# Performance work log

Measured on AMD Instinct MI355X. Metric: run time of the kernel, lower is better.

The kernel has to match this reference:

```python
import jax, jax.numpy as jnp
import numpy as np
from jax import lax

B, C_IN, C_OUT, N, R, K = 16, 64, 64, 32768, 32, 3
GROUPS, GN_EPS = 8, 1e-5


def swish(x):
    return x * jax.nn.sigmoid(x)


def group_norm(x, gamma, beta):
    b, c = x.shape[:2]
    xg = x.reshape(b, GROUPS, -1)
    mu = xg.mean(-1, keepdims=True)
    var = xg.var(-1, keepdims=True)
    xn = ((xg - mu) * lax.rsqrt(var + GN_EPS)).reshape(x.shape)
    shp = (1, c) + (1,) * (x.ndim - 2)
    return xn * gamma.reshape(shp) + beta.reshape(shp)


def conv3d(x, w, b):
    y = lax.conv_general_dilated(x, w, (1, 1, 1), 'SAME',
                                 dimension_numbers=('NCDHW', 'OIDHW', 'NCDHW'))
    return y + b.reshape(1, -1, 1, 1, 1)


def voxelize(features, coords):
    # features [B,C,N], coords [B,3,N] -> vox [B,C,R,R,R], norm_coords [B,3,N] in [0,R-1]
    c = coords - coords.mean(axis=2, keepdims=True)
    scale = jnp.linalg.norm(c, axis=1, keepdims=True).max(axis=2, keepdims=True) * 2.0  # eps=0
    norm = jnp.clip((c / scale + 0.5) * R, 0.0, R - 1)
    vc = jnp.round(norm).astype(jnp.int32)
    idx = (vc[:, 0] * R + vc[:, 1]) * R + vc[:, 2]  # [B,N] flat voxel index

    def per_batch(f, i):  # f [C,N], i [N] -> [C, R^3] scatter-average
        sums = jax.ops.segment_sum(f.T, i, num_segments=R ** 3)  # [R^3, C]
        cnt = jax.ops.segment_sum(jnp.ones(i.shape, f.dtype), i, num_segments=R ** 3)
        return (sums / jnp.maximum(cnt, 1.0)[:, None]).T

    vox = jax.vmap(per_batch)(features, idx).reshape(features.shape[0], features.shape[1], R, R, R)
    return vox, norm


def trilinear_devoxelize(vox, coords):
    # vox [B,C,R,R,R], coords [B,3,N] float in [0,R-1] -> [B,C,N]
    b, c = vox.shape[:2]
    flat = vox.reshape(b, c, R ** 3)
    c0f = jnp.floor(coords)
    f = coords - c0f
    i0 = jnp.clip(c0f.astype(jnp.int32), 0, R - 1)
    i1 = jnp.clip(i0 + 1, 0, R - 1)
    out = jnp.zeros((b, c, coords.shape[2]), vox.dtype)
    for xi, wx in ((i0[:, 0], 1.0 - f[:, 0]), (i1[:, 0], f[:, 0])):
        for yi, wy in ((i0[:, 1], 1.0 - f[:, 1]), (i1[:, 1], f[:, 1])):
            for zi, wz in ((i0[:, 2], 1.0 - f[:, 2]), (i1[:, 2], f[:, 2])):
                idx = (xi * R + yi) * R + zi  # [B,N]
                w = (wx * wy * wz)[:, None, :]
                out = out + jnp.take_along_axis(flat, idx[:, None, :], axis=2) * w
    return out


def setup_inputs():
    key = jax.random.key(0)
    ks = jax.random.split(key, 6)
    s1 = 1.0 / np.sqrt(C_IN * K ** 3)
    s2 = 1.0 / np.sqrt(C_OUT * K ** 3)
    sp = 1.0 / np.sqrt(C_IN)
    return {
        'features': jax.random.normal(ks[0], (B, C_IN, N), jnp.float32),
        'coords': jax.random.normal(ks[1], (B, 3, N), jnp.float32),
        'w1': jax.random.normal(ks[2], (C_OUT, C_IN, K, K, K), jnp.float32) * s1,
        'b1': jnp.zeros((C_OUT,), jnp.float32),
        'g1': jnp.ones((C_OUT,), jnp.float32),
        'be1': jnp.zeros((C_OUT,), jnp.float32),
        'w2': jax.random.normal(ks[3], (C_OUT, C_OUT, K, K, K), jnp.float32) * s2,
        'b2': jnp.zeros((C_OUT,), jnp.float32),
        'g2': jnp.ones((C_OUT,), jnp.float32),
        'be2': jnp.zeros((C_OUT,), jnp.float32),
        'wp': jax.random.normal(ks[4], (C_OUT, C_IN), jnp.float32) * sp,
        'bp': jnp.zeros((C_OUT,), jnp.float32),
        'gp': jnp.ones((C_OUT,), jnp.float32),
        'bep': jnp.zeros((C_OUT,), jnp.float32),
    }


def reference(features, coords, w1, b1, g1, be1, w2, b2, g2, be2, wp, bp, gp, bep):
    coords_sg = lax.stop_gradient(coords)  # torch: coords.detach() inside Voxelization
    vox, norm_coords = voxelize(features, coords_sg)
    h = swish(group_norm(conv3d(vox, w1, b1), g1, be1))
    # Dropout(0.1) is identity in eval mode
    h = swish(group_norm(conv3d(h, w2, b2), g2, be2))
    vpts = trilinear_devoxelize(h, norm_coords)
    pf = swish(group_norm(jnp.einsum('oc,bcn->bon', wp, features) + bp[None, :, None], gp, bep))
    return (vpts + pf, coords)
```

## Files before the change

kernel.cpp:

```cpp
#include <hip/hip_runtime.h>
#include <hip/hip_bf16.h>
#include <math.h>

#define BB   16
#define CCH  64
#define NPT  32768
#define RR   32
#define R3   32768
#define GSZ  262144
#define VOXB 2228224

typedef __attribute__((ext_vector_type(8))) short bfx8;
typedef __attribute__((ext_vector_type(8))) unsigned short usx8;
typedef __attribute__((ext_vector_type(16))) float f32x16;

__device__ __forceinline__ short f2bf(float f) {
    unsigned u = __builtin_bit_cast(unsigned, f);
    u += 0x7fff + ((u >> 16) & 1);
    return (short)(u >> 16);
}
__device__ __forceinline__ float bf2f(unsigned short s) {
    unsigned u = ((unsigned)s) << 16;
    return __builtin_bit_cast(float, u);
}

__device__ __forceinline__ int fzswz(int z) {
    return (((z & 3) ^ ((z >> 2) & 3)) << 3);
}

__device__ __forceinline__ float blockReduceSumF(float v) {
    __shared__ float sm[16];
    #pragma unroll
    for (int o = 32; o > 0; o >>= 1) v += __shfl_down(v, o);
    __syncthreads();
    if ((threadIdx.x & 63) == 0) sm[threadIdx.x >> 6] = v;
    __syncthreads();
    float s = 0.f;
    int nw = blockDim.x >> 6;
    for (int i = 0; i < nw; ++i) s += sm[i];
    return s;
}

__device__ __forceinline__ float blockReduceMaxF(float v) {
    __shared__ float sm[16];
    #pragma unroll
    for (int o = 32; o > 0; o >>= 1) v = fmaxf(v, __shfl_down(v, o));
    __syncthreads();
    if ((threadIdx.x & 63) == 0) sm[threadIdx.x >> 6] = v;
    __syncthreads();
    float s = sm[0];
    int nw = blockDim.x >> 6;
    for (int i = 1; i < nw; ++i) s = fmaxf(s, sm[i]);
    return s;
}

__global__ void k_cstat_sum(const float* __restrict__ coords, float* __restrict__ csum) {
    int b = blockIdx.x >> 3, seg = blockIdx.x & 7;
    const float* cb = coords + (size_t)b * 3 * NPT;
    int n0 = seg << 12;
    float sx = 0.f, sy = 0.f, sz = 0.f;
    for (int n = n0 + threadIdx.x; n < n0 + 4096; n += 256) {
        sx += cb[n]; sy += cb[NPT + n]; sz += cb[2 * NPT + n];
    }
    sx = blockReduceSumF(sx);
    sy = blockReduceSumF(sy);
    sz = blockReduceSumF(sz);
    if (threadIdx.x == 0) {
        atomicAdd(&csum[b * 4 + 0], sx);
        atomicAdd(&csum[b * 4 + 1], sy);
        atomicAdd(&csum[b * 4 + 2], sz);
    }
}

__global__ void k_cstat_max(const float* __restrict__ coords, const float* __restrict__ csum,
                            int* __restrict__ cmax) {
    int b = blockIdx.x >> 3, seg = blockIdx.x & 7;
    const float* cb = coords + (size_t)b * 3 * NPT;
    float mx = csum[b * 4 + 0] * (1.f / NPT);
    float my = csum[b * 4 + 1] * (1.f / NPT);
    float mz = csum[b * 4 + 2] * (1.f / NPT);
    int n0 = seg << 12;
    float mn = 0.f;
    for (int n = n0 + threadIdx.x; n < n0 + 4096; n += 256) {
        float x = cb[n] - mx, y = cb[NPT + n] - my, z = cb[2 * NPT + n] - mz;
        mn = fmaxf(mn, sqrtf(x * x + y * y + z * z));
    }
    mn = blockReduceMaxF(mn);
    if (threadIdx.x == 0) atomicMax(&cmax[b], __float_as_int(mn));
}

__global__ void k_norm_idx(const float* __restrict__ coords, const float* __restrict__ csum,
                           const int* __restrict__ cmax,
                           float* __restrict__ normc, int* __restrict__ vidx,
                           int* __restrict__ hist, float* __restrict__ out2) {
    int t = blockIdx.x * 256 + threadIdx.x;
    int b = t >> 15, n = t & 32767;
    float mx = csum[b * 4 + 0] * (1.f / NPT);
    float my = csum[b * 4 + 1] * (1.f / NPT);
    float mz = csum[b * 4 + 2] * (1.f / NPT);
    float scale = 2.f * __int_as_float(cmax[b]);
    const float* cb = coords + (size_t)b * 3 * NPT;
    float x = cb[n], y = cb[NPT + n], z = cb[2 * NPT + n];
    float nx = fminf(fmaxf(((x - mx) / scale + 0.5f) * 32.f, 0.f), 31.f);
    float ny = fminf(fmaxf(((y - my) / scale + 0.5f) * 32.f, 0.f), 31.f);
    float nz = fminf(fmaxf(((z - mz) / scale + 0.5f) * 32.f, 0.f), 31.f);
    float* nb = normc + (size_t)b * 3 * NPT;
    nb[n] = nx; nb[NPT + n] = ny; nb[2 * NPT + n] = nz;
    int vx = (int)rintf(nx), vy = (int)rintf(ny), vz = (int)rintf(nz);
    int v = (vx * 32 + vy) * 32 + vz;
    vidx[t] = v;
    atomicAdd(&hist[(b << 15) + v], 1);
    float* o2 = out2 + (size_t)b * 3 * NPT;
    o2[n] = x; o2[NPT + n] = y; o2[2 * NPT + n] = z;
}

__global__ __launch_bounds__(1024) void k_prefix(const int* __restrict__ hist,
                                                 int* __restrict__ startB,
                                                 int* __restrict__ base) {
    int b = blockIdx.x;
    int tid = threadIdx.x;
    const int* h = hist + (b << 15);
    int loc[32];
    int s = 0;
    #pragma unroll
    for (int j = 0; j < 32; ++j) { loc[j] = h[tid * 32 + j]; s += loc[j]; }
    __shared__ int sm[1024];
    sm[tid] = s;
    __syncthreads();
    for (int o = 1; o < 1024; o <<= 1) {
        int v = (tid >= o) ? sm[tid - o] : 0;
        __syncthreads();
        sm[tid] += v;
        __syncthreads();
    }
    int run = (tid ? sm[tid - 1] : 0);
    #pragma unroll
    for (int j = 0; j < 32; ++j) {
        int idx = (b << 15) + tid * 32 + j;
        startB[idx] = run;
        base[idx] = run;
        run += loc[j];
    }
}

__global__ __launch_bounds__(256) void k_reorder(const float* __restrict__ feat,
                                                 const int* __restrict__ vidx,
                                                 int* __restrict__ base,
                                                 short* __restrict__ featT) {
    __shared__ float tile[64][65];
    __shared__ int sslot[64];
    int blk = blockIdx.x;
    int b = blk >> 9;
    int n0 = (blk & 511) << 6;
    int tid = threadIdx.x;
    const float* fb = feat + ((size_t)b << 21);
    for (int e = tid; e < 64 * 16; e += 256) {
        int c = e >> 4, n4 = e & 15;
        float4 v4 = *(const float4*)(fb + ((size_t)c << 15) + n0 + n4 * 4);
        tile[c][n4 * 4 + 0] = v4.x; tile[c][n4 * 4 + 1] = v4.y;
        tile[c][n4 * 4 + 2] = v4.z; tile[c][n4 * 4 + 3] = v4.w;
    }
    if (tid < 64) {
        int v = vidx[(b << 15) + n0 + tid];
        sslot[tid] = atomicAdd(&base[(b << 15) + v], 1);
    }
    __syncthreads();
    int p = tid >> 2, q = tid & 3;
    int slot = sslot[p];
    short* dst = featT + (((size_t)((b << 15) + slot)) << 6) + q * 16;
    unsigned pk[8];
    #pragma unroll
    for (int k = 0; k < 8; ++k) {
        unsigned lo16 = (unsigned short)f2bf(tile[q * 16 + 2 * k][p]);
        unsigned hi16 = (unsigned short)f2bf(tile[q * 16 + 2 * k + 1][p]);
        pk[k] = lo16 | (hi16 << 16);
    }
    *(int4*)dst = make_int4(pk[0], pk[1], pk[2], pk[3]);
    *(int4*)(dst + 8) = make_int4(pk[4], pk[5], pk[6], pk[7]);
}

__global__ void k_vox_accum(const short* __restrict__ featT, const int* __restrict__ startB,
                            const int* __restrict__ base, short* __restrict__ vout) {
    int t = blockIdx.x * 256 + threadIdx.x;
    int lane4 = t & 15;
    int v = (t >> 4) & 32767;
    int b = t >> 19;
    int start = startB[(b << 15) + v];
    int end   = base[(b << 15) + v];
    float4 acc = make_float4(0.f, 0.f, 0.f, 0.f);
    const short* fT = featT + (((size_t)b << 15) << 6) + lane4 * 4;
    for (int p = start; p < end; ++p) {
        short4 hv = *(const short4*)(fT + ((size_t)p << 6));
        acc.x += bf2f((unsigned short)hv.x);
        acc.y += bf2f((unsigned short)hv.y);
        acc.z += bf2f((unsigned short)hv.z);
        acc.w += bf2f((unsigned short)hv.w);
    }
    float rc = 1.f / fmaxf((float)(end - start), 1.f);
    short4 pk;
    pk.x = f2bf(acc.x * rc); pk.y = f2bf(acc.y * rc);
    pk.z = f2bf(acc.z * rc); pk.w = f2bf(acc.w * rc);
    *(short4*)(vout + (size_t)b * VOXB + ((size_t)(v >> 5) * 34 + (v & 31) + 1) * 64 + lane4 * 4) = pk;
}

__global__ void k_padzero(short* __restrict__ v) {
    int t = blockIdx.x * 256 + threadIdx.x;
    int q = t & 7, zp = (t >> 3) & 1, xy = (t >> 4) & 1023, b = t >> 14;
    int z = zp ? 33 : 0;
    *(int4*)(v + (size_t)b * VOXB + ((size_t)xy * 34 + z) * 64 + q * 8) = make_int4(0, 0, 0, 0);
}

__global__ void k_wprep2(const float* __restrict__ w1, const float* __restrict__ w2,
                         short* __restrict__ wT1, short* __restrict__ wT2) {
    int e = blockIdx.x * 256 + threadIdx.x;
    const float* w = (e < 110592) ? w1 : w2;
    short* o = (e < 110592) ? wT1 : wT2;
    int ee = (e < 110592) ? e : e - 110592;
    int ci = ee & 63, co = (ee >> 6) & 63, k = ee >> 12;
    o[ee] = f2bf(w[(size_t)(co * 64 + ci) * 27 + k]);
}

template<bool FUSE>
__global__ __launch_bounds__(512, 4) void k_conv_mfma(
    const short* __restrict__ vin, const short* __restrict__ wT,
    const float* __restrict__ bias,
    const float* __restrict__ stin, const float* __restrict__ gin,
    const float* __restrict__ bein,
    short* __restrict__ vout, float* __restrict__ st)
{
    __shared__ short lds[36 * 1088];
    __shared__ float sred[8][2];
    int bid = blockIdx.x;
    int xcd = bid & 7, sub = bid >> 3;
    int b = (xcd << 1) | (sub >> 6);
    int tile = sub & 63;
    int x0 = (tile >> 3) << 2, y0 = (tile & 7) << 2;
    int tid = threadIdx.x;
    int wv8 = tid >> 6;
    int cb = wv8 & 1, xl = wv8 >> 1;
    int l = tid & 63, lo = l & 31, hi = l >> 5;
    const short* vb = vin + (size_t)b * VOXB;
    int xo = x0 + xl;
    if (tid < 16) ((float*)sred)[tid] = 0.f;

    f32x16 acc[4];
    #pragma unroll
    for (int j = 0; j < 4; ++j)
        #pragma unroll
        for (int i = 0; i < 16; ++i) acc[j][i] = 0.f;

    #pragma unroll
    for (int h = 0; h < 2; ++h) {
        if (h) __syncthreads();
        #pragma unroll
        for (int it = 0; it < 9; ++it) {
            int e = it * 512 + tid;
            int line = e >> 7, r = e & 127;
            int z = r >> 2, q = r & 3;
            int xx = line / 6, yy = line - xx * 6;
            int xi = x0 + xx - 1, yi = y0 + yy - 1;
            bool inb = ((unsigned)xi < 32u) && ((unsigned)yi < 32u);
            int4 v = make_int4(0, 0, 0, 0);
            if (inb)
                v = *(const int4*)(vb + ((size_t)(xi * 32 + yi) * 34 + z) * 64 + h * 32 + q * 8);
            if (FUSE) {
                if (inb && z >= 1) {
                    int ci0 = h * 32 + q * 8, cg = ci0 >> 3;
                    float s = stin[((b << 3) + cg) * 2 + 0];
                    float s2 = stin[((b << 3) + cg) * 2 + 1];
                    float mean = s * (1.f / 262144.f);
                    float rstd = rsqrtf(s2 * (1.f / 262144.f) - mean * mean + 1e-5f);
                    float4 ga = *(const float4*)(gin + ci0);
                    float4 gb = *(const float4*)(gin + ci0 + 4);
                    float4 ba = *(const float4*)(bein + ci0);
                    float4 bb = *(const float4*)(bein + ci0 + 4);
                    float gm[8] = {ga.x, ga.y, ga.z, ga.w, gb.x, gb.y, gb.z, gb.w};
                    float bt[8] = {ba.x, ba.y, ba.z, ba.w, bb.x, bb.y, bb.z, bb.w};
                    unsigned short* hv = (unsigned short*)&v;
                    #pragma unroll
                    for (int i = 0; i < 8; ++i) {
                        float f = bf2f(hv[i]);
                        float g = (f - mean) * rstd * gm[i] + bt[i];
                        float sw = g / (1.f + __expf(-g));
                        hv[i] = (unsigned short)f2bf(sw);
                    }
                }
            }
            int dst = line * 1088 + z * 32 + ((q * 8) ^ fzswz(z));
            *(int4*)(lds + dst) = v;
        }
        if (tid < 288) {
            int line = tid >> 3, rq = tid & 7;
            int z = 32 + (rq >> 2), q = rq & 3;
            int xx = line / 6, yy = line - xx * 6;
            int xi = x0 + xx - 1, yi = y0 + yy - 1;
            bool inb = ((unsigned)xi < 32u) && ((unsigned)yi < 32u);
            int4 v = make_int4(0, 0, 0, 0);
            if (inb)
                v = *(const int4*)(vb + ((size_t)(xi * 32 + yi) * 34 + z) * 64 + h * 32 + q * 8);
            if (FUSE) {
                if (inb && z <= 32) {
                    int ci0 = h * 32 + q * 8, cg = ci0 >> 3;
                    float s = stin[((b << 3) + cg) * 2 + 0];
                    float s2 = stin[((b << 3) + cg) * 2 + 1];
                    float mean = s * (1.f / 262144.f);
                    float rstd = rsqrtf(s2 * (1.f / 262144.f) - mean * mean + 1e-5f);
                    float4 ga = *(const float4*)(gin + ci0);
                    float4 gb = *(const float4*)(gin + ci0 + 4);
                    float4 ba = *(const float4*)(bein + ci0);
                    float4 bb = *(const float4*)(bein + ci0 + 4);
                    float gm[8] = {ga.x, ga.y, ga.z, ga.w, gb.x, gb.y, gb.z, gb.w};
                    float bt[8] = {ba.x, ba.y, ba.z, ba.w, bb.x, bb.y, bb.z, bb.w};
                    unsigned short* hv = (unsigned short*)&v;
                    #pragma unroll
                    for (int i = 0; i < 8; ++i) {
                        float f = bf2f(hv[i]);
                        float g = (f - mean) * rstd * gm[i] + bt[i];
                        float sw = g / (1.f + __expf(-g));
                        hv[i] = (unsigned short)f2bf(sw);
                    }
                }
            }
            int dst = line * 1088 + z * 32 + ((q * 8) ^ fzswz(z));
            *(int4*)(lds + dst) = v;
        }
        __syncthreads();
        const short* wbase = wT + lo * 64 + h * 32 + hi * 8 + cb * 2048;
        #pragma unroll
        for (int dx = 0; dx < 3; ++dx) {
            const short* ldsx = lds + ((xl + dx) * 6) * 1088;
            #pragma unroll
            for (int dz = 0; dz < 3; ++dz) {
                int zz = lo + dz;
                int swz = fzswz(zz);
                const short* bcol = ldsx + zz * 32;
                #pragma unroll
                for (int s = 0; s < 2; ++s) {
                    int slot = (s * 16 + hi * 8) ^ swz;
                    const short* wt0 = wbase + (dx * 9 + dz) * 4096 + s * 16;
                    bfx8 w0 = *(const bfx8*)(wt0);
                    bfx8 w1 = *(const bfx8*)(wt0 + 3 * 4096);
                    bfx8 w2 = *(const bfx8*)(wt0 + 6 * 4096);
                    #pragma unroll
                    for (int L = 0; L < 6; ++L) {
                        bfx8 bv = *(const bfx8*)(bcol + L * 1088 + slot);
                        if (L <= 3)
                            acc[L] = __builtin_amdgcn_mfma_f32_32x32x16_bf16(w0, bv, acc[L], 0, 0, 0);
                        if (L >= 1 && L <= 4)
                            acc[L-1] = __builtin_amdgcn_mfma_f32_32x32x16_bf16(w1, bv, acc[L-1], 0, 0, 0);
                        if (L >= 2)
                            acc[L-2] = __builtin_amdgcn_mfma_f32_32x32x16_bf16(w2, bv, acc[L-2], 0, 0, 0);
                    }
                }
            }
        }
    }

    float gs[4], gs2[4];
    #pragma unroll
    for (int g = 0; g < 4; ++g) { gs[g] = 0.f; gs2[g] = 0.f; }
    short* ob = vout + (size_t)b * VOXB;
    #pragma unroll
    for (int j = 0; j < 4; ++j) {
        size_t rb = ((size_t)(xo * 32 + y0 + j) * 34 + 1 + lo) * 64;
        #pragma unroll
        for (int q = 0; q < 4; ++q) {
            int co0 = cb * 32 + hi * 4 + q * 8;
            float v0 = acc[j][q * 4 + 0] + bias[co0 + 0];
            float v1 = acc[j][q * 4 + 1] + bias[co0 + 1];
            float v2 = acc[j][q * 4 + 2] + bias[co0 + 2];
            float v3 = acc[j][q * 4 + 3] + bias[co0 + 3];
            gs[q] += v0 + v1 + v2 + v3;
            gs2[q] += v0 * v0 + v1 * v1 + v2 * v2 + v3 * v3;
            short4 pk;
            pk.x = f2bf(v0); pk.y = f2bf(v1); pk.z = f2bf(v2); pk.w = f2bf(v3);
            *(short4*)(ob + rb + co0) = pk;
        }
    }
    #pragma unroll
    for (int q = 0; q < 4; ++q) {
        float s = gs[q], s2 = gs2[q];
        #pragma unroll
        for (int o = 32; o > 0; o >>= 1) { s += __shfl_down(s, o); s2 += __shfl_down(s2, o); }
        if (l == 0) { atomicAdd(&sred[cb * 4 + q][0], s); atomicAdd(&sred[cb * 4 + q][1], s2); }
    }
    __syncthreads();
    if (tid < 8) {
        atomicAdd(&st[((b << 3) + tid) * 2 + 0], sred[tid][0]);
        atomicAdd(&st[((b << 3) + tid) * 2 + 1], sred[tid][1]);
    }
}

__global__ __launch_bounds__(256) void k_point(const float* __restrict__ feat,
                                               const float* __restrict__ wp,
                                               const float* __restrict__ bp,
                                               short* __restrict__ pbuf,
                                               float* __restrict__ stp) {
    __shared__ float s_f[64][64];
    __shared__ float s_w[64][68];
    __shared__ float sred[8][2];
    int nblk = blockIdx.x * 64;
    int b = blockIdx.y;
    int tid = threadIdx.x;
    if (tid < 16) ((float*)sred)[tid] = 0.f;
    const float* fb = feat + (((size_t)b * CCH) << 15);
    for (int e = tid; e < 64 * 64; e += 256) {
        int c = e >> 6, nn = e & 63;
        s_f[c][nn] = fb[(((size_t)c) << 15) + nblk + nn];
        s_w[nn][c] = wp[e];
    }
    __syncthreads();
    int o0 = (tid >> 4) << 2;
    int n0 = (tid & 15) << 2;
    float acc[4][4] = {{0.f}};
    for (int c = 0; c < 64; ++c) {
        float4 fv = *(const float4*)&s_f[c][n0];
        float4 wv = *(const float4*)&s_w[c][o0];
        float fvv[4] = {fv.x, fv.y, fv.z, fv.w};
        float wvv[4] = {wv.x, wv.y, wv.z, wv.w};
        #pragma unroll
        for (int j = 0; j < 4; ++j)
            #pragma unroll
            for (int i = 0; i < 4; ++i) acc[j][i] += wvv[j] * fvv[i];
    }
    float s = 0.f, s2 = 0.f;
    #pragma unroll
    for (int j = 0; j < 4; ++j) {
        float bb = bp[o0 + j];
        short* op = pbuf + (((size_t)(b * CCH + o0 + j)) << 15) + nblk + n0;
        short4 pk;
        float v0 = acc[j][0] + bb, v1 = acc[j][1] + bb;
        float v2 = acc[j][2] + bb, v3 = acc[j][3] + bb;
        s += v0 + v1 + v2 + v3;
        s2 += v0 * v0 + v1 * v1 + v2 * v2 + v3 * v3;
        pk.x = f2bf(v0); pk.y = f2bf(v1); pk.z = f2bf(v2); pk.w = f2bf(v3);
        *(short4*)op = pk;
    }
    int g = o0 >> 3;
    atomicAdd(&sred[g][0], s);
    atomicAdd(&sred[g][1], s2);
    __syncthreads();
    if (tid < 8) {
        atomicAdd(&stp[(b * 8 + tid) * 2 + 0], sred[tid][0]);
        atomicAdd(&stp[(b * 8 + tid) * 2 + 1], sred[tid][1]);
    }
}

__global__ __launch_bounds__(256) void k_final(
    const short* __restrict__ h, const float* __restrict__ normc,
    const float* __restrict__ st2, const float* __restrict__ g2v,
    const float* __restrict__ be2v,
    const float* __restrict__ stp, const float* __restrict__ gp,
    const float* __restrict__ bep, const short* __restrict__ pbuf,
    float* __restrict__ out1) {
    __shared__ float sm[64][33];
    int tid = threadIdx.x;
    int s = tid & 7, pp = tid >> 3;
    int blk = blockIdx.x;
    int b = blk >> 10;
    int n0 = (blk & 1023) << 5;
    int n = n0 + pp;
    const float* nb = normc + (size_t)b * 3 * NPT;
    float nx = nb[n], ny = nb[NPT + n], nz = nb[2 * NPT + n];
    float fxf = floorf(nx), fyf = floorf(ny), fzf = floorf(nz);
    float fx = nx - fxf, fy = ny - fyf, fz = nz - fzf;
    int x0 = (int)fxf; x0 = x0 < 31 ? x0 : 31;
    int y0 = (int)fyf; y0 = y0 < 31 ? y0 : 31;
    int z0 = (int)fzf; z0 = z0 < 31 ? z0 : 31;
    int x1 = x0 + 1 < 31 ? x0 + 1 : 31;
    int y1 = y0 + 1 < 31 ? y0 + 1 : 31;
    int z1 = z0 + 1 < 31 ? z0 + 1 : 31;
    float wx0 = 1.f - fx, wx1 = fx, wy0 = 1.f - fy, wy1 = fy, wz0 = 1.f - fz, wz1 = fz;

    float s2m = st2[(b * 8 + s) * 2 + 0], s2q = st2[(b * 8 + s) * 2 + 1];
    float mean2 = s2m * (1.f / 262144.f);
    float rstd2 = rsqrtf(s2q * (1.f / 262144.f) - mean2 * mean2 + 1e-5f);
    float scl[8], sft[8];
    #pragma unroll
    for (int i = 0; i < 8; ++i) {
        float gmm = g2v[s * 8 + i];
        scl[i] = gmm * rstd2;
        sft[i] = be2v[s * 8 + i] - mean2 * gmm * rstd2;
    }

    const short* hb = h + (size_t)b * VOXB + s * 8;
    float acc[8];
    #pragma unroll
    for (int i = 0; i < 8; ++i) acc[i] = 0.f;
    #pragma unroll
    for (int cx = 0; cx < 2; ++cx) {
        int xi = cx ? x1 : x0; float wxx = cx ? wx1 : wx0;
        #pragma unroll
        for (int cy = 0; cy < 2; ++cy) {
            int yi = cy ? y1 : y0; float wyy = cy ? wy1 : wy0;
            #pragma unroll
            for (int cz = 0; cz < 2; ++cz) {
                int zi = cz ? z1 : z0; float wzz = cz ? wz1 : wz0;
                float w = wxx * wyy * wzz;
                usx8 hv = *(const usx8*)(hb + ((size_t)(xi * 32 + yi) * 34 + zi + 1) * 64);
                #pragma unroll
                for (int i = 0; i < 8; ++i) {
                    float g = bf2f(hv[i]) * scl[i] + sft[i];
                    float sw = g / (1.f + __expf(-g));
                    acc[i] = fmaf(w, sw, acc[i]);
                }
            }
        }
    }
    float ss = stp[(b * 8 + s) * 2 + 0], ss2 = stp[(b * 8 + s) * 2 + 1];
    float mean = ss * (1.f / 262144.f);
    float rstd = rsqrtf(ss2 * (1.f / 262144.f) - mean * mean + 1e-5f);
    const short* pb = pbuf + (((size_t)(b * CCH)) << 15) + n;
    #pragma unroll
    for (int i = 0; i < 8; ++i) {
        int co = s * 8 + i;
        float pv = bf2f((unsigned short)pb[((size_t)co) << 15]);
        float g = (pv - mean) * rstd * gp[co] + bep[co];
        float sw = g / (1.f + __expf(-g));
        sm[co][pp] = acc[i] + sw;
    }
    __syncthreads();
    int co = tid >> 2, q = (tid & 3) << 3;
    float r0 = sm[co][q + 0], r1 = sm[co][q + 1], r2 = sm[co][q + 2], r3 = sm[co][q + 3];
    float r4 = sm[co][q + 4], r5 = sm[co][q + 5], r6 = sm[co][q + 6], r7 = sm[co][q + 7];
    float* op = out1 + (((size_t)(b * CCH + co)) << 15) + n0 + q;
    *(float4*)op = make_float4(r0, r1, r2, r3);
    *(float4*)(op + 4) = make_float4(r4, r5, r6, r7);
}

extern "C" void kernel_launch(void* const* d_in, const int* in_sizes, int n_in,
                              void* d_out, int out_size, void* d_ws, size_t ws_size,
                              hipStream_t stream) {
    const float* feat   = (const float*)d_in[0];
    const float* coords = (const float*)d_in[1];
    const float* w1  = (const float*)d_in[2];
    const float* b1  = (const float*)d_in[3];
    const float* g1  = (const float*)d_in[4];
    const float* be1 = (const float*)d_in[5];
    const float* w2  = (const float*)d_in[6];
    const float* b2  = (const float*)d_in[7];
    const float* g2  = (const float*)d_in[8];
    const float* be2 = (const float*)d_in[9];
    const float* wp  = (const float*)d_in[10];
    const float* bp  = (const float*)d_in[11];
    const float* gp  = (const float*)d_in[12];
    const float* bep = (const float*)d_in[13];

    float* out1 = (float*)d_out;
    float* out2 = out1 + (size_t)BB * CCH * NPT;

    const size_t reg0Bytes = (size_t)BB * NPT * CCH * 4;
    short* featT    = (short*)d_ws;
    short* voxT_mid = (short*)d_ws;
    short* pbuf     = (short*)d_ws;
    short* voxT_in  = (short*)((char*)d_ws + reg0Bytes);
    char* p = (char*)voxT_in + (size_t)BB * VOXB * 2;
    int*   hist   = (int*)p;  p += (size_t)BB * R3 * 4;
    int*   startB = (int*)p;  p += (size_t)BB * R3 * 4;
    int*   base   = (int*)p;  p += (size_t)BB * R3 * 4;
    float* normc = (float*)p; p += (size_t)BB * 3 * NPT * 4;
    int*   vidx  = (int*)p;   p += (size_t)BB * NPT * 4;
    short* wT1   = (short*)p; p += 110592 * 2;
    short* wT2   = (short*)p; p += 110592 * 2;
    float* st1   = (float*)p; p += 256 * 4;
    float* st2   = (float*)p; p += 256 * 4;
    float* stp   = (float*)p; p += 256 * 4;
    float* csum  = (float*)p; p += 64 * 4;
    int*   cmax  = (int*)p;   p += 16 * 4;

    hipMemsetAsync(hist, 0, (size_t)BB * R3 * 4, stream);
    hipMemsetAsync(st1, 0, (256 * 3 + 64 + 16) * 4, stream);

    k_padzero<<<1024, 256, 0, stream>>>(voxT_in);
    k_cstat_sum<<<128, 256, 0, stream>>>(coords, csum);
    k_cstat_max<<<128, 256, 0, stream>>>(coords, csum, cmax);
    k_norm_idx<<<(BB * NPT) / 256, 256, 0, stream>>>(coords, csum, cmax, normc, vidx, hist, out2);
    k_prefix<<<BB, 1024, 0, stream>>>(hist, startB, base);
    k_reorder<<<(BB * NPT) / 64, 256, 0, stream>>>(feat, vidx, base, featT);
    k_vox_accum<<<(BB * R3 * 16) / 256, 256, 0, stream>>>(featT, startB, base, voxT_in);
    k_wprep2<<<864, 256, 0, stream>>>(w1, w2, wT1, wT2);

    k_padzero<<<1024, 256, 0, stream>>>(voxT_mid);

    k_conv_mfma<false><<<1024, 512, 0, stream>>>(voxT_in, wT1, b1,
                                                 nullptr, nullptr, nullptr, voxT_mid, st1);
    k_conv_mfma<true><<<1024, 512, 0, stream>>>(voxT_mid, wT2, b2,
                                                st1, g1, be1, voxT_in, st2);

    k_point<<<dim3(NPT / 64, BB), 256, 0, stream>>>(feat, wp, bp, pbuf, stp);

    k_final<<<(BB * NPT) / 32, 256, 0, stream>>>(voxT_in, normc, st2, g2, be2,
                                                 stp, gp, bep, pbuf, out1);
}
```

Measured before the change: 746.7 us.

## Split voxel accumulation across two lanes, precompute GN affine, transpose point buffer

The voxel scatter-average now splits each voxel's point list between two thread halves and merges them with a lane shuffle, which halves the serial loop length for dense voxels. A small kernel folds GroupNorm statistics, gamma and beta into per-(batch,channel) scale and shift. Both conv2's fused input normalisation and the final kernel now read those values instead of recomputing mean and rstd per element group. The point-branch buffer changes from channel-major to point-major layout, so the final kernel reads 8 channels with one vector load instead of 8 strided scalar loads. The cost is two extra tiny launches and twice as many threads in the accumulation kernel.

```diff
diff --git a/kernel.cpp b/kernel.cpp
--- a/kernel.cpp
+++ b/kernel.cpp
@@ -183,24 +183,31 @@
                             const int* __restrict__ base, short* __restrict__ vout) {
     int t = blockIdx.x * 256 + threadIdx.x;
     int lane4 = t & 15;
-    int v = (t >> 4) & 32767;
-    int b = t >> 19;
+    int ph = (t >> 4) & 1;
+    int v = (t >> 5) & 32767;
+    int b = t >> 20;
     int start = startB[(b << 15) + v];
     int end   = base[(b << 15) + v];
     float4 acc = make_float4(0.f, 0.f, 0.f, 0.f);
     const short* fT = featT + (((size_t)b << 15) << 6) + lane4 * 4;
-    for (int p = start; p < end; ++p) {
+    for (int p = start + ph; p < end; p += 2) {
         short4 hv = *(const short4*)(fT + ((size_t)p << 6));
         acc.x += bf2f((unsigned short)hv.x);
         acc.y += bf2f((unsigned short)hv.y);
         acc.z += bf2f((unsigned short)hv.z);
         acc.w += bf2f((unsigned short)hv.w);
     }
-    float rc = 1.f / fmaxf((float)(end - start), 1.f);
-    short4 pk;
-    pk.x = f2bf(acc.x * rc); pk.y = f2bf(acc.y * rc);
-    pk.z = f2bf(acc.z * rc); pk.w = f2bf(acc.w * rc);
-    *(short4*)(vout + (size_t)b * VOXB + ((size_t)(v >> 5) * 34 + (v & 31) + 1) * 64 + lane4 * 4) = pk;
+    acc.x += __shfl_xor(acc.x, 16);
+    acc.y += __shfl_xor(acc.y, 16);
+    acc.z += __shfl_xor(acc.z, 16);
+    acc.w += __shfl_xor(acc.w, 16);
+    if (ph == 0) {
+        float rc = 1.f / fmaxf((float)(end - start), 1.f);
+        short4 pk;
+        pk.x = f2bf(acc.x * rc); pk.y = f2bf(acc.y * rc);
+        pk.z = f2bf(acc.z * rc); pk.w = f2bf(acc.w * rc);
+        *(short4*)(vout + (size_t)b * VOXB + ((size_t)(v >> 5) * 34 + (v & 31) + 1) * 64 + lane4 * 4) = pk;
+    }
 }
 
 __global__ void k_padzero(short* __restrict__ v) {
@@ -220,12 +227,24 @@
     o[ee] = f2bf(w[(size_t)(co * 64 + ci) * 27 + k]);
 }
 
+__global__ void k_gnprep(const float* __restrict__ st, const float* __restrict__ g,
+                         const float* __restrict__ be,
+                         float* __restrict__ scl, float* __restrict__ sft) {
+    int t = blockIdx.x * 256 + threadIdx.x;
+    int b = t >> 6, c = t & 63, cg = c >> 3;
+    float s = st[(b * 8 + cg) * 2 + 0], s2 = st[(b * 8 + cg) * 2 + 1];
+    float mean = s * (1.f / 262144.f);
+    float rstd = rsqrtf(s2 * (1.f / 262144.f) - mean * mean + 1e-5f);
+    float gm = g[c];
+    scl[t] = gm * rstd;
+    sft[t] = be[c] - mean * gm * rstd;
+}
+
 template<bool FUSE>
 __global__ __launch_bounds__(512, 4) void k_conv_mfma(
     const short* __restrict__ vin, const short* __restrict__ wT,
     const float* __restrict__ bias,
-    const float* __restrict__ stin, const float* __restrict__ gin,
-    const float* __restrict__ bein,
+    const float* __restrict__ scl, const float* __restrict__ sft,
     short* __restrict__ vout, float* __restrict__ st)
 {
     __shared__ short lds[36 * 1088];
@@ -265,22 +284,17 @@
                 v = *(const int4*)(vb + ((size_t)(xi * 32 + yi) * 34 + z) * 64 + h * 32 + q * 8);
             if (FUSE) {
                 if (inb && z >= 1) {
-                    int ci0 = h * 32 + q * 8, cg = ci0 >> 3;
-                    float s = stin[((b << 3) + cg) * 2 + 0];
-                    float s2 = stin[((b << 3) + cg) * 2 + 1];
-                    float mean = s * (1.f / 262144.f);
-                    float rstd = rsqrtf(s2 * (1.f / 262144.f) - mean * mean + 1e-5f);
-                    float4 ga = *(const float4*)(gin + ci0);
-                    float4 gb = *(const float4*)(gin + ci0 + 4);
-                    float4 ba = *(const float4*)(bein + ci0);
-                    float4 bb = *(const float4*)(bein + ci0 + 4);
-                    float gm[8] = {ga.x, ga.y, ga.z, ga.w, gb.x, gb.y, gb.z, gb.w};
-                    float bt[8] = {ba.x, ba.y, ba.z, ba.w, bb.x, bb.y, bb.z, bb.w};
+                    int ci0 = (b << 6) + h * 32 + q * 8;
+                    float4 sa = *(const float4*)(scl + ci0);
+                    float4 sb = *(const float4*)(scl + ci0 + 4);
+                    float4 fa = *(const float4*)(sft + ci0);
+                    float4 fb = *(const float4*)(sft + ci0 + 4);
+                    float sv[8] = {sa.x, sa.y, sa.z, sa.w, sb.x, sb.y, sb.z, sb.w};
+                    float fv[8] = {fa.x, fa.y, fa.z, fa.w, fb.x, fb.y, fb.z, fb.w};
                     unsigned short* hv = (unsigned short*)&v;
                     #pragma unroll
                     for (int i = 0; i < 8; ++i) {
-                        float f = bf2f(hv[i]);
-                        float g = (f - mean) * rstd * gm[i] + bt[i];
+                        float g = fmaf(bf2f(hv[i]), sv[i], fv[i]);
                         float sw = g / (1.f + __expf(-g));
                         hv[i] = (unsigned short)f2bf(sw);
                     }
@@ -300,22 +314,17 @@
                 v = *(const int4*)(vb + ((size_t)(xi * 32 + yi) * 34 + z) * 64 + h * 32 + q * 8);
             if (FUSE) {
                 if (inb && z <= 32) {
-                    int ci0 = h * 32 + q * 8, cg = ci0 >> 3;
-                    float s = stin[((b << 3) + cg) * 2 + 0];
-                    float s2 = stin[((b << 3) + cg) * 2 + 1];
-                    float mean = s * (1.f / 262144.f);
-                    float rstd = rsqrtf(s2 * (1.f / 262144.f) - mean * mean + 1e-5f);
-                    float4 ga = *(const float4*)(gin + ci0);
-                    float4 gb = *(const float4*)(gin + ci0 + 4);
-                    float4 ba = *(const float4*)(bein + ci0);
-                    float4 bb = *(const float4*)(bein + ci0 + 4);
-                    float gm[8] = {ga.x, ga.y, ga.z, ga.w, gb.x, gb.y, gb.z, gb.w};
-                    float bt[8] = {ba.x, ba.y, ba.z, ba.w, bb.x, bb.y, bb.z, bb.w};
+                    int ci0 = (b << 6) + h * 32 + q * 8;
+                    float4 sa = *(const float4*)(scl + ci0);
+                    float4 sb = *(const float4*)(scl + ci0 + 4);
+                    float4 fa = *(const float4*)(sft + ci0);
+                    float4 fb = *(const float4*)(sft + ci0 + 4);
+                    float sv[8] = {sa.x, sa.y, sa.z, sa.w, sb.x, sb.y, sb.z, sb.w};
+                    float fv[8] = {fa.x, fa.y, fa.z, fa.w, fb.x, fb.y, fb.z, fb.w};
                     unsigned short* hv = (unsigned short*)&v;
                     #pragma unroll
                     for (int i = 0; i < 8; ++i) {
-                        float f = bf2f(hv[i]);
-                        float g = (f - mean) * rstd * gm[i] + bt[i];
+                        float g = fmaf(bf2f(hv[i]), sv[i], fv[i]);
                         float sw = g / (1.f + __expf(-g));
                         hv[i] = (unsigned short)f2bf(sw);
                     }
@@ -423,18 +432,17 @@
             #pragma unroll
             for (int i = 0; i < 4; ++i) acc[j][i] += wvv[j] * fvv[i];
     }
+    float bb0 = bp[o0], bb1 = bp[o0 + 1], bb2 = bp[o0 + 2], bb3 = bp[o0 + 3];
     float s = 0.f, s2 = 0.f;
     #pragma unroll
-    for (int j = 0; j < 4; ++j) {
-        float bb = bp[o0 + j];
-        short* op = pbuf + (((size_t)(b * CCH + o0 + j)) << 15) + nblk + n0;
-        short4 pk;
-        float v0 = acc[j][0] + bb, v1 = acc[j][1] + bb;
-        float v2 = acc[j][2] + bb, v3 = acc[j][3] + bb;
+    for (int i = 0; i < 4; ++i) {
+        float v0 = acc[0][i] + bb0, v1 = acc[1][i] + bb1;
+        float v2 = acc[2][i] + bb2, v3 = acc[3][i] + bb3;
         s += v0 + v1 + v2 + v3;
         s2 += v0 * v0 + v1 * v1 + v2 * v2 + v3 * v3;
+        short4 pk;
         pk.x = f2bf(v0); pk.y = f2bf(v1); pk.z = f2bf(v2); pk.w = f2bf(v3);
-        *(short4*)op = pk;
+        *(short4*)(pbuf + (((size_t)((b << 15) + nblk + n0 + i)) << 6) + o0) = pk;
     }
     int g = o0 >> 3;
     atomicAdd(&sred[g][0], s);
@@ -448,8 +456,7 @@
 
 __global__ __launch_bounds__(256) void k_final(
     const short* __restrict__ h, const float* __restrict__ normc,
-    const float* __restrict__ st2, const float* __restrict__ g2v,
-    const float* __restrict__ be2v,
+    const float* __restrict__ scl2, const float* __restrict__ sft2,
     const float* __restrict__ stp, const float* __restrict__ gp,
     const float* __restrict__ bep, const short* __restrict__ pbuf,
     float* __restrict__ out1) {
@@ -472,15 +479,17 @@
     int z1 = z0 + 1 < 31 ? z0 + 1 : 31;
     float wx0 = 1.f - fx, wx1 = fx, wy0 = 1.f - fy, wy1 = fy, wz0 = 1.f - fz, wz1 = fz;
 
-    float s2m = st2[(b * 8 + s) * 2 + 0], s2q = st2[(b * 8 + s) * 2 + 1];
-    float mean2 = s2m * (1.f / 262144.f);
-    float rstd2 = rsqrtf(s2q * (1.f / 262144.f) - mean2 * mean2 + 1e-5f);
     float scl[8], sft[8];
-    #pragma unroll
-    for (int i = 0; i < 8; ++i) {
-        float gmm = g2v[s * 8 + i];
-        scl[i] = gmm * rstd2;
-        sft[i] = be2v[s * 8 + i] - mean2 * gmm * rstd2;
+    {
+        int ci0 = (b << 6) + s * 8;
+        float4 sa = *(const float4*)(scl2 + ci0);
+        float4 sb = *(const float4*)(scl2 + ci0 + 4);
+        float4 fa = *(const float4*)(sft2 + ci0);
+        float4 fb = *(const float4*)(sft2 + ci0 + 4);
+        scl[0] = sa.x; scl[1] = sa.y; scl[2] = sa.z; scl[3] = sa.w;
+        scl[4] = sb.x; scl[5] = sb.y; scl[6] = sb.z; scl[7] = sb.w;
+        sft[0] = fa.x; sft[1] = fa.y; sft[2] = fa.z; sft[3] = fa.w;
+        sft[4] = fb.x; sft[5] = fb.y; sft[6] = fb.z; sft[7] = fb.w;
     }
 
     const short* hb = h + (size_t)b * VOXB + s * 8;
@@ -500,7 +509,7 @@
                 usx8 hv = *(const usx8*)(hb + ((size_t)(xi * 32 + yi) * 34 + zi + 1) * 64);
                 #pragma unroll
                 for (int i = 0; i < 8; ++i) {
-                    float g = bf2f(hv[i]) * scl[i] + sft[i];
+                    float g = fmaf(bf2f(hv[i]), scl[i], sft[i]);
                     float sw = g / (1.f + __expf(-g));
                     acc[i] = fmaf(w, sw, acc[i]);
                 }
@@ -510,11 +519,11 @@
     float ss = stp[(b * 8 + s) * 2 + 0], ss2 = stp[(b * 8 + s) * 2 + 1];
     float mean = ss * (1.f / 262144.f);
     float rstd = rsqrtf(ss2 * (1.f / 262144.f) - mean * mean + 1e-5f);
-    const short* pb = pbuf + (((size_t)(b * CCH)) << 15) + n;
+    usx8 pv8 = *(const usx8*)(pbuf + (((size_t)((b << 15) + n)) << 6) + s * 8);
     #pragma unroll
     for (int i = 0; i < 8; ++i) {
         int co = s * 8 + i;
-        float pv = bf2f((unsigned short)pb[((size_t)co) << 15]);
+        float pv = bf2f(pv8[i]);
         float g = (pv - mean) * rstd * gp[co] + bep[co];
         float sw = g / (1.f + __expf(-g));
         sm[co][pp] = acc[i] + sw;
@@ -567,6 +576,10 @@
     float* stp   = (float*)p; p += 256 * 4;
     float* csum  = (float*)p; p += 64 * 4;
     int*   cmax  = (int*)p;   p += 16 * 4;
+    float* scl1  = (float*)p; p += 1024 * 4;
+    float* sft1  = (float*)p; p += 1024 * 4;
+    float* scl2  = (float*)p; p += 1024 * 4;
+    float* sft2  = (float*)p; p += 1024 * 4;
 
     hipMemsetAsync(hist, 0, (size_t)BB * R3 * 4, stream);
     hipMemsetAsync(st1, 0, (256 * 3 + 64 + 16) * 4, stream);
@@ -577,18 +590,20 @@
     k_norm_idx<<<(BB * NPT) / 256, 256, 0, stream>>>(coords, csum, cmax, normc, vidx, hist, out2);
     k_prefix<<<BB, 1024, 0, stream>>>(hist, startB, base);
     k_reorder<<<(BB * NPT) / 64, 256, 0, stream>>>(feat, vidx, base, featT);
-    k_vox_accum<<<(BB * R3 * 16) / 256, 256, 0, stream>>>(featT, startB, base, voxT_in);
+    k_vox_accum<<<(BB * R3 * 32) / 256, 256, 0, stream>>>(featT, startB, base, voxT_in);
     k_wprep2<<<864, 256, 0, stream>>>(w1, w2, wT1, wT2);
 
     k_padzero<<<1024, 256, 0, stream>>>(voxT_mid);
 
     k_conv_mfma<false><<<1024, 512, 0, stream>>>(voxT_in, wT1, b1,
-                                                 nullptr, nullptr, nullptr, voxT_mid, st1);
+                                                 nullptr, nullptr, voxT_mid, st1);
+    k_gnprep<<<4, 256, 0, stream>>>(st1, g1, be1, scl1, sft1);
     k_conv_mfma<true><<<1024, 512, 0, stream>>>(voxT_mid, wT2, b2,
-                                                st1, g1, be1, voxT_in, st2);
+                                                scl1, sft1, voxT_in, st2);
+    k_gnprep<<<4, 256, 0, stream>>>(st2, g2, be2, scl2, sft2);
 
     k_point<<<dim3(NPT / 64, BB), 256, 0, stream>>>(feat, wp, bp, pbuf, stp);
 
-    k_final<<<(BB * NPT) / 32, 256, 0, stream>>>(voxT_in, normc, st2, g2, be2,
+    k_final<<<(BB * NPT) / 32, 256, 0, stream>>>(voxT_in, normc, scl2, sft2,
                                                  stp, gp, bep, pbuf, out1);
 }
```

New measurement: 737.5 us. Within noise of the previous version (-1.2%).
